# Optimization experiments

Hardware: AMD Instinct MI355X
Metric: run time of the kernel (lower is better)

Reference implementation:

```python
import jax, jax.numpy as jnp
import numpy as np

FRAME, PROJ, MID, HID, T, B = 2048, 512, 128, 1024, 48, 512


def _uniform(key, shape, stdv):
    return jax.random.uniform(key, shape, jnp.float32, -stdv, stdv)


def setup_inputs() -> dict:
    key = jax.random.key(0)
    ks = jax.random.split(key, 16)
    sp = 1.0 / np.sqrt(FRAME)   # frame_embed init
    s1 = 1.0 / np.sqrt(HID)     # LSTMCell init (1/sqrt(hidden))
    sbd = 1.0 / np.sqrt(PROJ)   # BoundaryDetector init (1/sqrt(i_features))
    return {
        "video_feats": jax.random.normal(ks[0], (B, T, FRAME), jnp.float32),
        # frame_embed: Linear(frame_size, projected_size)
        "We": _uniform(ks[1], (PROJ, FRAME), sp),
        "be": _uniform(ks[2], (PROJ,), sp),
        # lstm1: LSTMCell(projected, hidden) with bias
        "W1_ih": _uniform(ks[3], (4 * HID, PROJ), s1),
        "W1_hh": _uniform(ks[4], (4 * HID, HID), s1),
        "b1_ih": _uniform(ks[5], (4 * HID,), s1),
        "b1_hh": _uniform(ks[6], (4 * HID,), s1),
        # lstm2: LSTMCell(hidden, hidden), bias=False
        "W2_ih": _uniform(ks[7], (4 * HID, HID), s1),
        "W2_hh": _uniform(ks[8], (4 * HID, HID), s1),
        # BoundaryDetector params
        "Wsi": _uniform(ks[9], (MID, PROJ), sbd),
        "Wsh": _uniform(ks[10], (MID, HID), sbd),
        "bbd": _uniform(ks[11], (MID,), sbd),
        "vs": _uniform(ks[12], (1, MID), sbd),
    }


def _lstm_cell(x, h, c, W_ih, W_hh, b):
    gates = x @ W_ih.T + h @ W_hh.T + b  # [B, 4H]
    i, f, g, o = jnp.split(gates, 4, axis=-1)  # PyTorch gate order i,f,g,o
    i, f, o = jax.nn.sigmoid(i), jax.nn.sigmoid(f), jax.nn.sigmoid(o)
    g = jnp.tanh(g)
    c_new = f * c + i * g
    h_new = o * jnp.tanh(c_new)
    return h_new, c_new


def _binary_gate(z):
    # eval mode: threshold 0.5; straight-through identity backward
    hard = (z > 0.5).astype(z.dtype)
    return z + jax.lax.stop_gradient(hard - z)


def reference(video_feats, We, be, W1_ih, W1_hh, b1_ih, b1_hh, W2_ih, W2_hh, Wsi, Wsh, bbd, vs):
    bsz = video_feats.shape[0]
    # frame embedding (dropout is identity in eval mode)
    v = video_feats @ We.T + be  # [B, T, PROJ]
    v_t = jnp.swapaxes(v, 0, 1)  # [T, B, PROJ]
    b1 = b1_ih + b1_hh
    zeros = jnp.zeros((bsz, HID), video_feats.dtype)

    def step(carry, vt):
        h1, c1, h2, c2 = carry
        z = jax.nn.sigmoid((vt @ Wsi.T + h1 @ Wsh.T + bbd) @ vs.T)  # [B, 1]
        s = _binary_gate(z)
        h1n, c1n = _lstm_cell(vt, h1, c1, W1_ih, W1_hh, b1)
        h2n, c2n = _lstm_cell(h1n * s, h2, c2, W2_ih, W2_hh, 0.0)
        h1n = h1n * (1.0 - s)
        c1n = c1n * (1.0 - s)
        return (h1n, c1n, h2n, c2n), None

    (h1, _, _, _), _ = jax.lax.scan(step, (zeros, zeros, zeros, zeros), v_t)
    return h1
```

## Files before the change

### kernel.cpp

```cpp
#include <hip/hip_runtime.h>

#define B_     512
#define T_     48
#define FRAME_ 2048
#define PROJ_  512
#define MID_   128
#define HID_   1024
#define G4_    4096

typedef unsigned short u16;
typedef __bf16 bf16x8 __attribute__((ext_vector_type(8)));
typedef float  f32x4  __attribute__((ext_vector_type(4)));

__device__ __forceinline__ float sigmoidf_(float x) {
    return 1.0f / (1.0f + expf(-x));
}
__device__ __forceinline__ u16 f2bf_rn(float f) {
    unsigned int u = __float_as_uint(f);
    u += 0x7fffu + ((u >> 16) & 1u);
    return (u16)(u >> 16);
}
__device__ __forceinline__ float bf2f(u16 s) {
    return __uint_as_float(((unsigned int)s) << 16);
}
__device__ __forceinline__ void gld16(const void* g, void* l) {
    __builtin_amdgcn_global_load_lds((const __attribute__((address_space(1))) void*)g,
                                     (__attribute__((address_space(3))) void*)l, 16, 0, 0);
}
__device__ __forceinline__ uint4 pack8(const u16* h) {
    return make_uint4((unsigned)h[0] | ((unsigned)h[1] << 16),
                      (unsigned)h[2] | ((unsigned)h[3] << 16),
                      (unsigned)h[4] | ((unsigned)h[5] << 16),
                      (unsigned)h[6] | ((unsigned)h[7] << 16));
}

__global__ void wvec_kernel(const float* __restrict__ Wsi, const float* __restrict__ Wsh,
                            const float* __restrict__ vs,
                            double* __restrict__ wsi_vd, float* __restrict__ wsh_v)
{
    const int gid = blockIdx.x * 256 + threadIdx.x;
    if (gid < 512) {
        double s = 0.0;
        for (int mi = 0; mi < MID_; ++mi)
            s += (double)vs[mi] * (double)Wsi[(size_t)mi * PROJ_ + gid];
        wsi_vd[gid] = s;
    } else if (gid < 1536) {
        const int k = gid - 512;
        double s = 0.0;
        for (int mi = 0; mi < MID_; ++mi)
            s += (double)vs[mi] * (double)Wsh[(size_t)mi * HID_ + k];
        wsh_v[k] = (float)s;
    }
}

__global__ void cc_kernel(const float* __restrict__ be, const double* __restrict__ wsi_vd,
                          const float* __restrict__ vs, const float* __restrict__ bbd,
                          double* __restrict__ cc)
{
    __shared__ double red[256];
    const int tid = threadIdx.x;
    double s = 0.0;
    for (int p = tid; p < PROJ_; p += 256) s += (double)be[p] * wsi_vd[p];
    red[tid] = s;
    __syncthreads();
    for (int st = 128; st > 0; st >>= 1) {
        if (tid < st) red[tid] += red[tid + st];
        __syncthreads();
    }
    if (tid == 0) {
        double b = 0.0;
        for (int mi = 0; mi < MID_; ++mi) b += (double)vs[mi] * (double)bbd[mi];
        cc[0] = red[0] + b;
    }
}

__global__ void u_kernel(const float* __restrict__ We, const double* __restrict__ wsi_vd,
                         double* __restrict__ u)
{
    const int f = blockIdx.x * 256 + threadIdx.x;
    double s = 0.0;
    for (int p = 0; p < PROJ_; ++p)
        s += wsi_vd[p] * (double)We[(size_t)p * FRAME_ + f];
    u[f] = s;
}

__global__ __launch_bounds__(256)
void vidpack_kernel(const float* __restrict__ video, const double* __restrict__ u,
                    const double* __restrict__ cc,
                    u16* __restrict__ phi, u16* __restrict__ plo,
                    float* __restrict__ Lv)
{
    __shared__ double red[16][17];
    const int tid = threadIdx.x;
    const int r   = tid & 15, kq = tid >> 4;
    const int row = blockIdx.x * 16 + r;
    const float* vr = video + (size_t)row * FRAME_;
    double s = 0.0;
#pragma unroll
    for (int j = 0; j < 16; ++j) {
        const int k0 = kq * 128 + j * 8;
        const float4 a = *(const float4*)&vr[k0];
        const float4 b = *(const float4*)&vr[k0 + 4];
        const float f[8] = {a.x, a.y, a.z, a.w, b.x, b.y, b.z, b.w};
        s += (double)f[0]*u[k0+0] + (double)f[1]*u[k0+1] + (double)f[2]*u[k0+2]
           + (double)f[3]*u[k0+3] + (double)f[4]*u[k0+4] + (double)f[5]*u[k0+5]
           + (double)f[6]*u[k0+6] + (double)f[7]*u[k0+7];
        u16 h[8], l[8];
#pragma unroll
        for (int e = 0; e < 8; ++e) {
            h[e] = f2bf_rn(f[e]);
            l[e] = f2bf_rn(f[e] - bf2f(h[e]));
        }
        const int g = kq * 16 + j;
        const size_t off = ((size_t)g * 24576 + row) * 16;
        *(uint4*)((char*)phi + off) = pack8(h);
        *(uint4*)((char*)plo + off) = pack8(l);
    }
    red[r][kq] = s;
    __syncthreads();
    if (tid < 16) {
        double t = 0.0;
#pragma unroll
        for (int q = 0; q < 16; ++q) t += red[tid][q];
        const int rw = blockIdx.x * 16 + tid;
        Lv[(rw % T_) * B_ + rw / T_] = (float)(t + cc[0]);
    }
}

__global__ void wepack_kernel(const float* __restrict__ We,
                              u16* __restrict__ phi, u16* __restrict__ plo)
{
    const int kk = blockIdx.x, by = blockIdx.y, tid = threadIdx.x;
#pragma unroll
    for (int pass = 0; pass < 2; ++pass) {
        const int g = tid + pass * 256;
        const int ko = g >> 7, n = g & 127;
        const int p = by * 128 + n;
        const int k = kk * 32 + ko * 8;
        const float4 a = *(const float4*)&We[(size_t)p * FRAME_ + k];
        const float4 b = *(const float4*)&We[(size_t)p * FRAME_ + k + 4];
        const float f[8] = {a.x, a.y, a.z, a.w, b.x, b.y, b.z, b.w};
        u16 h[8], l[8];
#pragma unroll
        for (int e = 0; e < 8; ++e) {
            h[e] = f2bf_rn(f[e]);
            l[e] = f2bf_rn(f[e] - bf2f(h[e]));
        }
        const size_t off = (((size_t)by * 64 + kk) * 512 + g) * 16;
        *(uint4*)((char*)phi + off) = pack8(h);
        *(uint4*)((char*)plo + off) = pack8(l);
    }
}

__global__ void wihpack_kernel(const float* __restrict__ Wih,
                               u16* __restrict__ phi, u16* __restrict__ plo)
{
    const int kk = blockIdx.x, by = blockIdx.y, tid = threadIdx.x;
#pragma unroll
    for (int pass = 0; pass < 2; ++pass) {
        const int g = tid + pass * 256;
        const int ko = g >> 7, n = g & 127;
        const int gate = n & 3, hl = n >> 2;
        const int srow = gate * HID_ + by * 32 + hl;
        const int k = kk * 32 + ko * 8;
        const float4 a = *(const float4*)&Wih[(size_t)srow * PROJ_ + k];
        const float4 b = *(const float4*)&Wih[(size_t)srow * PROJ_ + k + 4];
        const float f[8] = {a.x, a.y, a.z, a.w, b.x, b.y, b.z, b.w};
        u16 h[8], l[8];
#pragma unroll
        for (int e = 0; e < 8; ++e) {
            h[e] = f2bf_rn(f[e]);
            l[e] = f2bf_rn(f[e] - bf2f(h[e]));
        }
        const size_t off = (((size_t)by * 16 + kk) * 512 + g) * 16;
        *(uint4*)((char*)phi + off) = pack8(h);
        *(uint4*)((char*)plo + off) = pack8(l);
    }
}

__global__ void whhpack_kernel(const float* __restrict__ Whh,
                               u16* __restrict__ phi, u16* __restrict__ plo)
{
    const int kk = blockIdx.x, by = blockIdx.y, tid = threadIdx.x;
#pragma unroll
    for (int pass = 0; pass < 2; ++pass) {
        const int g = tid + pass * 256;
        const int ko = g >> 7, n = g & 127;
        const int gate = n & 3, hl = n >> 2;
        const int srow = gate * HID_ + by * 32 + hl;
        const int k = kk * 32 + ko * 8;
        const float4 a = *(const float4*)&Whh[(size_t)srow * HID_ + k];
        const float4 b = *(const float4*)&Whh[(size_t)srow * HID_ + k + 4];
        const float f[8] = {a.x, a.y, a.z, a.w, b.x, b.y, b.z, b.w};
        u16 h[8], l[8];
#pragma unroll
        for (int e = 0; e < 8; ++e) {
            h[e] = f2bf_rn(f[e]);
            l[e] = f2bf_rn(f[e] - bf2f(h[e]));
        }
        const size_t off = (((size_t)by * 32 + kk) * 512 + g) * 16;
        *(uint4*)((char*)phi + off) = pack8(h);
        *(uint4*)((char*)plo + off) = pack8(l);
    }
}

__global__ void b1g_kernel(const float* __restrict__ bih, const float* __restrict__ bhh,
                           float* __restrict__ b1g)
{
    const int n = blockIdx.x * 256 + threadIdx.x;
    const int by = n >> 7, nl = n & 127;
    const int gate = nl & 3, hl = nl >> 2;
    const int src = gate * HID_ + by * 32 + hl;
    b1g[n] = bih[src] + bhh[src];
}


__global__ __launch_bounds__(512, 4)
void embed_mfma_kernel(const u16* __restrict__ Ahi_g, const u16* __restrict__ Alo_g,
                       const u16* __restrict__ Bhi_g, const u16* __restrict__ Blo_g,
                       const float* __restrict__ be,
                       u16* __restrict__ vphi, u16* __restrict__ vplo)
{
    __shared__ char smem[33792];
    const int tid = threadIdx.x;
    const int xcd = blockIdx.x & 7, s_ = blockIdx.x >> 3;
    const int by = s_ & 3, bx = xcd * 48 + (s_ >> 2);
    const int n0 = by * 128;
    const int w = tid >> 6, l = tid & 63, lm = l & 15, ko4 = l >> 4;
    const int wr = (w >> 2) * 32, wc = (w & 3) * 32;
    const int t8 = tid & 255;
    const int koA = t8 >> 6, am = t8 & 63;

    const char* aV = (const char*)(tid < 256 ? Ahi_g : Alo_g)
                     + (size_t)koA * 393216 + ((size_t)bx * 64 + am) * 16;
    const char* bh = (const char*)Bhi_g + (size_t)by * 524288
                     + ((size_t)(ko4 * 128 + wc + lm)) * 16;
    const char* bl = (const char*)Blo_g + (size_t)by * 524288
                     + ((size_t)(ko4 * 128 + wc + lm)) * 16;
    char* lbase = smem + (tid >> 8) * 4096 + t8 * 16;

    f32x4 acc[2][2] = {};
    bf16x8 nBh[2], nBl[2], cBh[2], cBl[2], fAh[2], fAl[2];

    gld16(aV, lbase);
    gld16(aV + 1572864, lbase + 8192);
#pragma unroll
    for (int nt = 0; nt < 2; ++nt) {
        nBh[nt] = *(const bf16x8*)(bh + nt * 256);
        nBl[nt] = *(const bf16x8*)(bl + nt * 256);
    }

#pragma unroll
    for (int kk = 0; kk < 64; ++kk) {
        if (kk == 63) asm volatile("s_waitcnt vmcnt(4)\ns_barrier" ::: "memory");
        else          asm volatile("s_waitcnt vmcnt(5)\ns_barrier" ::: "memory");
        __builtin_amdgcn_sched_barrier(0);
#pragma unroll
        for (int nt = 0; nt < 2; ++nt) { cBh[nt] = nBh[nt]; cBl[nt] = nBl[nt]; }
        const char* rb = smem + (kk & 3) * 8192;
#pragma unroll
        for (int mt = 0; mt < 2; ++mt) {
            fAh[mt] = *(const bf16x8*)(rb + (ko4 * 64 + wr + mt * 16 + lm) * 16);
            fAl[mt] = *(const bf16x8*)(rb + 4096 + (ko4 * 64 + wr + mt * 16 + lm) * 16);
        }
        if (kk + 1 < 64) {
#pragma unroll
            for (int nt = 0; nt < 2; ++nt) {
                nBh[nt] = *(const bf16x8*)(bh + (size_t)(kk + 1) * 8192 + nt * 256);
                nBl[nt] = *(const bf16x8*)(bl + (size_t)(kk + 1) * 8192 + nt * 256);
            }
        }
        if (kk + 2 < 64) gld16(aV + (size_t)(kk + 2) * 1572864, lbase + ((kk + 2) & 3) * 8192);
#pragma unroll
        for (int mt = 0; mt < 2; ++mt)
#pragma unroll
            for (int nt = 0; nt < 2; ++nt) {
                acc[mt][nt] = __builtin_amdgcn_mfma_f32_16x16x32_bf16(fAh[mt], cBh[nt], acc[mt][nt], 0, 0, 0);
                acc[mt][nt] = __builtin_amdgcn_mfma_f32_16x16x32_bf16(fAh[mt], cBl[nt], acc[mt][nt], 0, 0, 0);
                acc[mt][nt] = __builtin_amdgcn_mfma_f32_16x16x32_bf16(fAl[mt], cBh[nt], acc[mt][nt], 0, 0, 0);
            }
    }
    asm volatile("s_waitcnt lgkmcnt(0)" ::: "memory");
    __builtin_amdgcn_sched_barrier(0);

    __syncthreads();
    float* S = (float*)smem;
#pragma unroll
    for (int mt = 0; mt < 2; ++mt)
#pragma unroll
        for (int nt = 0; nt < 2; ++nt) {
            const int col = wc + nt * 16 + lm;
#pragma unroll
            for (int r = 0; r < 4; ++r) {
                const int row = wr + mt * 16 + ko4 * 4 + r;
                S[row * 132 + col] = acc[mt][nt][r];
            }
        }
    __syncthreads();

#pragma unroll
    for (int pass = 0; pass < 2; ++pass) {
        const int pidx = tid + pass * 512;
        const int m = pidx >> 4, gr = pidx & 15;
        const int p0 = n0 + gr * 8;
        const float4 s0 = *(const float4*)&S[m * 132 + gr * 8];
        const float4 s1 = *(const float4*)&S[m * 132 + gr * 8 + 4];
        const float4 e0 = *(const float4*)&be[p0];
        const float4 e1 = *(const float4*)&be[p0 + 4];
        const float o[8] = {s0.x + e0.x, s0.y + e0.y, s0.z + e0.z, s0.w + e0.w,
                            s1.x + e1.x, s1.y + e1.y, s1.z + e1.z, s1.w + e1.w};
        u16 h[8], lo[8];
#pragma unroll
        for (int e = 0; e < 8; ++e) {
            h[e] = f2bf_rn(o[e]);
            lo[e] = f2bf_rn(o[e] - bf2f(h[e]));
        }
        const int R = bx * 64 + m;
        const int t = R % T_, b = R / T_;
        const size_t off = (size_t)t * 524288 + (((size_t)(p0 >> 3)) * 512 + b) * 16;
        *(uint4*)((char*)vphi + off) = pack8(h);
        *(uint4*)((char*)vplo + off) = pack8(lo);
    }
}

__global__ __launch_bounds__(512, 4)
void gx_mfma_kernel(const u16* __restrict__ vphi, const u16* __restrict__ vplo,
                    const u16* __restrict__ Wihhi, const u16* __restrict__ Wihlo,
                    const float* __restrict__ b1g, float* __restrict__ Gx)
{
    __shared__ char smem[33792];
    const int tid = threadIdx.x;
    const int by32 = blockIdx.x & 31;
    const int tb2  = blockIdx.x >> 5;
    const int t2 = tb2 >> 3, bx2 = tb2 & 7;
    const int b02 = bx2 * 64, n02 = by32 * 128;
    const int w = tid >> 6, l = tid & 63, lm = l & 15, ko4 = l >> 4;
    const int wr = (w >> 2) * 32, wc = (w & 3) * 32;
    const int t8 = tid & 255;
    const int koA = t8 >> 6, am = t8 & 63;

    const char* aV = (const char*)(tid < 256 ? vphi : vplo)
                     + (size_t)t2 * 524288 + ((size_t)koA * 512 + b02 + am) * 16;
    const char* bh = (const char*)Wihhi + (size_t)by32 * 131072
                     + ((size_t)(ko4 * 128 + wc + lm)) * 16;
    const char* bl = (const char*)Wihlo + (size_t)by32 * 131072
                     + ((size_t)(ko4 * 128 + wc + lm)) * 16;
    char* lbase = smem + (tid >> 8) * 4096 + t8 * 16;

    f32x4 acc[2][2] = {};
    bf16x8 nBh[2], nBl[2], cBh[2], cBl[2], fAh[2], fAl[2];

    gld16(aV, lbase);
    gld16(aV + 32768, lbase + 8192);
#pragma unroll
    for (int nt = 0; nt < 2; ++nt) {
        nBh[nt] = *(const bf16x8*)(bh + nt * 256);
        nBl[nt] = *(const bf16x8*)(bl + nt * 256);
    }

#pragma unroll
    for (int kk = 0; kk < 16; ++kk) {
        if (kk == 15) asm volatile("s_waitcnt vmcnt(4)\ns_barrier" ::: "memory");
        else          asm volatile("s_waitcnt vmcnt(5)\ns_barrier" ::: "memory");
        __builtin_amdgcn_sched_barrier(0);
#pragma unroll
        for (int nt = 0; nt < 2; ++nt) { cBh[nt] = nBh[nt]; cBl[nt] = nBl[nt]; }
        const char* rb = smem + (kk & 3) * 8192;
#pragma unroll
        for (int mt = 0; mt < 2; ++mt) {
            fAh[mt] = *(const bf16x8*)(rb + (ko4 * 64 + wr + mt * 16 + lm) * 16);
            fAl[mt] = *(const bf16x8*)(rb + 4096 + (ko4 * 64 + wr + mt * 16 + lm) * 16);
        }
        if (kk + 1 < 16) {
#pragma unroll
            for (int nt = 0; nt < 2; ++nt) {
                nBh[nt] = *(const bf16x8*)(bh + (size_t)(kk + 1) * 8192 + nt * 256);
                nBl[nt] = *(const bf16x8*)(bl + (size_t)(kk + 1) * 8192 + nt * 256);
            }
        }
        if (kk + 2 < 16) gld16(aV + (size_t)(kk + 2) * 32768, lbase + ((kk + 2) & 3) * 8192);
#pragma unroll
        for (int mt = 0; mt < 2; ++mt)
#pragma unroll
            for (int nt = 0; nt < 2; ++nt) {
                acc[mt][nt] = __builtin_amdgcn_mfma_f32_16x16x32_bf16(fAh[mt], cBh[nt], acc[mt][nt], 0, 0, 0);
                acc[mt][nt] = __builtin_amdgcn_mfma_f32_16x16x32_bf16(fAh[mt], cBl[nt], acc[mt][nt], 0, 0, 0);
                acc[mt][nt] = __builtin_amdgcn_mfma_f32_16x16x32_bf16(fAl[mt], cBh[nt], acc[mt][nt], 0, 0, 0);
            }
    }
    asm volatile("s_waitcnt lgkmcnt(0)" ::: "memory");
    __builtin_amdgcn_sched_barrier(0);

    __syncthreads();
    float* S = (float*)smem;
#pragma unroll
    for (int mt = 0; mt < 2; ++mt)
#pragma unroll
        for (int nt = 0; nt < 2; ++nt) {
            const int col = wc + nt * 16 + lm;
#pragma unroll
            for (int r = 0; r < 4; ++r) {
                const int row = wr + mt * 16 + ko4 * 4 + r;
                S[row * 132 + col] = acc[mt][nt][r];
            }
        }
    __syncthreads();

#pragma unroll
    for (int pass = 0; pass < 2; ++pass) {
        const int pidx = tid + pass * 512;
        const int m = pidx >> 4, gr = pidx & 15;
        const int c0 = gr * 8;
        const float4 s0 = *(const float4*)&S[m * 132 + c0];
        const float4 s1 = *(const float4*)&S[m * 132 + c0 + 4];
        const float4 a0 = *(const float4*)&b1g[n02 + c0];
        const float4 a1 = *(const float4*)&b1g[n02 + c0 + 4];
        float* dst = Gx + ((size_t)t2 * 512 + b02 + m) * 4096 + n02 + c0;
        *(float4*)dst       = make_float4(s0.x + a0.x, s0.y + a0.y, s0.z + a0.z, s0.w + a0.w);
        *(float4*)(dst + 4) = make_float4(s1.x + a1.x, s1.y + a1.y, s1.z + a1.z, s1.w + a1.w);
    }
}

__global__ __launch_bounds__(512, 2)
void lstm_mfma_kernel(const u16* __restrict__ hhi,  const u16* __restrict__ hlo,
                      const u16* __restrict__ Whhhi, const u16* __restrict__ Whhlo,
                      const float* __restrict__ Gxt,
                      const float* __restrict__ Lv_t,
                      const float* __restrict__ Pin,
                      float* __restrict__ Pout,
                      const float* __restrict__ wsh_v,
                      float* __restrict__ c1, float* __restrict__ h1o,
                      u16* __restrict__ hhio, u16* __restrict__ hloo)
{
    __shared__ char smem[34048];
    float* keepsm = (float*)(smem + 33792);
    const int tid = threadIdx.x;
    const int bid = blockIdx.x;
    const int xcd = bid & 7, slot = bid >> 3;
    const int by  = xcd * 4 + (slot & 3);
    const int bx  = slot >> 2;
    const int b0  = bx * 64;
    const int w = tid >> 6, l = tid & 63, lm = l & 15, ko4 = l >> 4;
    const int wr = (w >> 2) * 32, wc = (w & 3) * 32;
    const int t8 = tid & 255;
    const int koA = t8 >> 6, am = t8 & 63;

    if (tid < 64) {
        double s = (double)Lv_t[b0 + tid];
#pragma unroll
        for (int j = 0; j < 32; ++j) s += (double)Pin[j * B_ + b0 + tid];
        keepsm[tid] = (s > 0.0) ? 0.0f : 1.0f;
    }

    const char* aH = (const char*)(tid < 256 ? hhi : hlo)
                     + ((size_t)koA * 512 + b0 + am) * 16;
    const char* bh = (const char*)Whhhi + (size_t)by * 262144
                     + ((size_t)(ko4 * 128 + wc + lm)) * 16;
    const char* bl = (const char*)Whhlo + (size_t)by * 262144
                     + ((size_t)(ko4 * 128 + wc + lm)) * 16;
    char* lbase = smem + (tid >> 8) * 4096 + t8 * 16;

    f32x4 acc[2][2] = {};
    bf16x8 nBh[2], nBl[2], cBh[2], cBl[2], fAh[2], fAl[2];

    gld16(aH, lbase);
    gld16(aH + 32768, lbase + 8192);
#pragma unroll
    for (int nt = 0; nt < 2; ++nt) {
        nBh[nt] = *(const bf16x8*)(bh + nt * 256);
        nBl[nt] = *(const bf16x8*)(bl + nt * 256);
    }

#pragma unroll
    for (int kk = 0; kk < 32; ++kk) {
        if (kk == 31) asm volatile("s_waitcnt vmcnt(4)\ns_barrier" ::: "memory");
        else          asm volatile("s_waitcnt vmcnt(5)\ns_barrier" ::: "memory");
        __builtin_amdgcn_sched_barrier(0);
#pragma unroll
        for (int nt = 0; nt < 2; ++nt) { cBh[nt] = nBh[nt]; cBl[nt] = nBl[nt]; }
        const char* rb = smem + (kk & 3) * 8192;
#pragma unroll
        for (int mt = 0; mt < 2; ++mt) {
            fAh[mt] = *(const bf16x8*)(rb + (ko4 * 64 + wr + mt * 16 + lm) * 16);
            fAl[mt] = *(const bf16x8*)(rb + 4096 + (ko4 * 64 + wr + mt * 16 + lm) * 16);
        }
        if (kk + 1 < 32) {
#pragma unroll
            for (int nt = 0; nt < 2; ++nt) {
                nBh[nt] = *(const bf16x8*)(bh + (size_t)(kk + 1) * 8192 + nt * 256);
                nBl[nt] = *(const bf16x8*)(bl + (size_t)(kk + 1) * 8192 + nt * 256);
            }
        }
        if (kk + 2 < 32) gld16(aH + (size_t)(kk + 2) * 32768, lbase + ((kk + 2) & 3) * 8192);
#pragma unroll
        for (int mt = 0; mt < 2; ++mt)
#pragma unroll
            for (int nt = 0; nt < 2; ++nt) {
                acc[mt][nt] = __builtin_amdgcn_mfma_f32_16x16x32_bf16(fAh[mt], cBh[nt], acc[mt][nt], 0, 0, 0);
                acc[mt][nt] = __builtin_amdgcn_mfma_f32_16x16x32_bf16(fAh[mt], cBl[nt], acc[mt][nt], 0, 0, 0);
                acc[mt][nt] = __builtin_amdgcn_mfma_f32_16x16x32_bf16(fAl[mt], cBh[nt], acc[mt][nt], 0, 0, 0);
            }
    }
    asm volatile("s_waitcnt lgkmcnt(0)" ::: "memory");
    __builtin_amdgcn_sched_barrier(0);

    const int h_l = tid & 31, rg = tid >> 5;
    const int hg  = by * 32 + h_l;
    float4 gx[4];
#pragma unroll
    for (int i = 0; i < 4; ++i)
        gx[i] = *(const float4*)&Gxt[((size_t)b0 + rg * 4 + i) * 4096 + by * 128 + h_l * 4];

    __syncthreads();
    float* S = (float*)smem;
#pragma unroll
    for (int mt = 0; mt < 2; ++mt)
#pragma unroll
        for (int nt = 0; nt < 2; ++nt) {
            const int col = wc + nt * 16 + lm;
#pragma unroll
            for (int r = 0; r < 4; ++r) {
                const int row = wr + mt * 16 + ko4 * 4 + r;
                S[row * 132 + col] = acc[mt][nt][r];
            }
        }
    __syncthreads();

    const float wv = wsh_v[hg];
    const size_t hgbase = (((size_t)by * 4 + (h_l >> 3)) * 512) * 16 + (h_l & 7) * 2;
#pragma unroll
    for (int i = 0; i < 4; ++i) {
        const int m = rg * 4 + i;
        const int b = b0 + m;
        const float4 g4 = *(const float4*)&S[m * 132 + h_l * 4];
        const float i_ = sigmoidf_(g4.x + gx[i].x);
        const float f_ = sigmoidf_(g4.y + gx[i].y);
        const float g_ = tanhf(g4.z + gx[i].z);
        const float o_ = sigmoidf_(g4.w + gx[i].w);
        const size_t off = (size_t)b * HID_ + hg;
        float cn = f_ * c1[off] + i_ * g_;
        float hn = o_ * tanhf(cn);
        const float kp = keepsm[m];
        cn *= kp; hn *= kp;
        c1[off] = cn;
        if (h1o) h1o[off] = hn;
        const u16 hb = f2bf_rn(hn);
        const size_t hoff = hgbase + (size_t)b * 16;
        *(u16*)((char*)hhio + hoff) = hb;
        *(u16*)((char*)hloo + hoff) = f2bf_rn(hn - bf2f(hb));
        float pr = hn * wv;
        pr += __shfl_xor(pr, 16);
        pr += __shfl_xor(pr, 8);
        pr += __shfl_xor(pr, 4);
        pr += __shfl_xor(pr, 2);
        pr += __shfl_xor(pr, 1);
        if (h_l == 0) Pout[by * B_ + b] = pr;
    }
}

extern "C" void kernel_launch(void* const* d_in, const int* in_sizes, int n_in,
                              void* d_out, int out_size, void* d_ws, size_t ws_size,
                              hipStream_t stream)
{
    const float* video = (const float*)d_in[0];
    const float* We    = (const float*)d_in[1];
    const float* be    = (const float*)d_in[2];
    const float* W1_ih = (const float*)d_in[3];
    const float* W1_hh = (const float*)d_in[4];
    const float* b1_ih = (const float*)d_in[5];
    const float* b1_hh = (const float*)d_in[6];
    const float* Wsi   = (const float*)d_in[9];
    const float* Wsh   = (const float*)d_in[10];
    const float* bbd   = (const float*)d_in[11];
    const float* vs    = (const float*)d_in[12];
    float* out = (float*)d_out;

    char* p = (char*)d_ws;
    auto alloc = [&](size_t bytes) { char* r = p; p += (bytes + 255) & ~(size_t)255; return r; };
    u16* vidhi = (u16*)alloc((size_t)24576 * FRAME_ * 2);
    u16* vidlo = (u16*)alloc((size_t)24576 * FRAME_ * 2);
    u16* vphi  = (u16*)alloc((size_t)T_ * B_ * PROJ_ * 2);
    u16* vplo  = (u16*)alloc((size_t)T_ * B_ * PROJ_ * 2);
    u16* Wehi  = (u16*)alloc((size_t)PROJ_ * FRAME_ * 2);
    u16* Welo  = (u16*)alloc((size_t)PROJ_ * FRAME_ * 2);
    u16* Wihhi = (u16*)alloc((size_t)G4_ * PROJ_ * 2);
    u16* Wihlo = (u16*)alloc((size_t)G4_ * PROJ_ * 2);
    u16* Whhhi = (u16*)alloc((size_t)G4_ * HID_ * 2);
    u16* Whhlo = (u16*)alloc((size_t)G4_ * HID_ * 2);
    float* Gx  = (float*)alloc((size_t)T_ * B_ * G4_ * 4);
    float* c1  = (float*)alloc((size_t)B_ * HID_ * 4);
    u16* hhiA  = (u16*)alloc((size_t)B_ * HID_ * 2);
    u16* hhiB  = (u16*)alloc((size_t)B_ * HID_ * 2);
    u16* hloA  = (u16*)alloc((size_t)B_ * HID_ * 2);
    u16* hloB  = (u16*)alloc((size_t)B_ * HID_ * 2);
    double* wsi_vd = (double*)alloc(512 * 8);
    double* ud     = (double*)alloc(2048 * 8);
    double* ccd    = (double*)alloc(256);
    float* wsh_v = (float*)alloc(1024 * 4);
    float* Lv    = (float*)alloc((size_t)T_ * B_ * 4);
    float* PA    = (float*)alloc(32 * B_ * 4);
    float* PB    = (float*)alloc(32 * B_ * 4);
    float* b1g   = (float*)alloc(G4_ * 4);

    hipMemsetAsync(c1,   0, (size_t)B_ * HID_ * 4, stream);
    hipMemsetAsync(hhiA, 0, (size_t)B_ * HID_ * 2, stream);
    hipMemsetAsync(hloA, 0, (size_t)B_ * HID_ * 2, stream);
    hipMemsetAsync(PA,   0, 32 * B_ * 4, stream);

    b1g_kernel<<<16, 256, 0, stream>>>(b1_ih, b1_hh, b1g);
    wvec_kernel<<<6, 256, 0, stream>>>(Wsi, Wsh, vs, wsi_vd, wsh_v);
    cc_kernel<<<1, 256, 0, stream>>>(be, wsi_vd, vs, bbd, ccd);
    u_kernel<<<8, 256, 0, stream>>>(We, wsi_vd, ud);
    wepack_kernel<<<dim3(64, 4), 256, 0, stream>>>(We, Wehi, Welo);
    wihpack_kernel<<<dim3(16, 32), 256, 0, stream>>>(W1_ih, Wihhi, Wihlo);
    whhpack_kernel<<<dim3(32, 32), 256, 0, stream>>>(W1_hh, Whhhi, Whhlo);
    vidpack_kernel<<<1536, 256, 0, stream>>>(video, ud, ccd, vidhi, vidlo, Lv);
    embed_mfma_kernel<<<1536, 512, 0, stream>>>(vidhi, vidlo, Wehi, Welo, be, vphi, vplo);
    gx_mfma_kernel<<<12288, 512, 0, stream>>>(vphi, vplo, Wihhi, Wihlo, b1g, Gx);

    u16* hhi_in = hhiA; u16* hhi_out = hhiB;
    u16* hlo_in = hloA; u16* hlo_out = hloB;
    float* Pin = PA; float* Pout = PB;

    for (int t = 0; t < T_; ++t) {
        float* ho = (t == T_ - 1) ? out : nullptr;
        lstm_mfma_kernel<<<256, 512, 0, stream>>>(hhi_in, hlo_in, Whhhi, Whhlo,
                                                  Gx + (size_t)t * B_ * G4_,
                                                  Lv + t * B_, Pin, Pout, wsh_v,
                                                  c1, ho, hhi_out, hlo_out);
        { u16* tmp = hhi_in; hhi_in = hhi_out; hhi_out = tmp; }
        { u16* tmp = hlo_in; hlo_in = hlo_out; hlo_out = tmp; }
        { float* tmp = Pin; Pin = Pout; Pout = tmp; }
    }
}
```

Measured before the change: 1.782 ms.

## Retile embed and Gx GEMMs to 128x128 with LDS-staged A and B

The embed and input-projection GEMMs move from 64x128 tiles on 512-thread blocks to 128x128 tiles on 256-thread blocks, each wave computing a 64x64 sub-tile. Both A and B operands are now staged through double-buffered LDS with async global loads, instead of B being read directly from global memory into registers. The Gx kernel writes results plus bias straight from registers, skipping the LDS transpose. The aim is more reuse per loaded byte and fewer redundant B fetches, at the cost of higher register and LDS use per block, which lowers occupancy.

```diff
diff --git a/kernel.cpp b/kernel.cpp
--- a/kernel.cpp
+++ b/kernel.cpp
@@ -215,210 +215,212 @@
 }
 
 
-__global__ __launch_bounds__(512, 4)
+__global__ __launch_bounds__(256, 2)
 void embed_mfma_kernel(const u16* __restrict__ Ahi_g, const u16* __restrict__ Alo_g,
                        const u16* __restrict__ Bhi_g, const u16* __restrict__ Blo_g,
                        const float* __restrict__ be,
                        u16* __restrict__ vphi, u16* __restrict__ vplo)
 {
-    __shared__ char smem[33792];
+    __shared__ char smem[65536];
     const int tid = threadIdx.x;
     const int xcd = blockIdx.x & 7, s_ = blockIdx.x >> 3;
-    const int by = s_ & 3, bx = xcd * 48 + (s_ >> 2);
-    const int n0 = by * 128;
+    const int by = s_ & 3, bx = xcd * 24 + (s_ >> 2);
+    const int n0 = by * 128, row0 = bx * 128;
     const int w = tid >> 6, l = tid & 63, lm = l & 15, ko4 = l >> 4;
-    const int wr = (w >> 2) * 32, wc = (w & 3) * 32;
-    const int t8 = tid & 255;
-    const int koA = t8 >> 6, am = t8 & 63;
-
-    const char* aV = (const char*)(tid < 256 ? Ahi_g : Alo_g)
-                     + (size_t)koA * 393216 + ((size_t)bx * 64 + am) * 16;
-    const char* bh = (const char*)Bhi_g + (size_t)by * 524288
-                     + ((size_t)(ko4 * 128 + wc + lm)) * 16;
-    const char* bl = (const char*)Blo_g + (size_t)by * 524288
-                     + ((size_t)(ko4 * 128 + wc + lm)) * 16;
-    char* lbase = smem + (tid >> 8) * 4096 + t8 * 16;
-
-    f32x4 acc[2][2] = {};
-    bf16x8 nBh[2], nBl[2], cBh[2], cBl[2], fAh[2], fAl[2];
-
-    gld16(aV, lbase);
-    gld16(aV + 1572864, lbase + 8192);
-#pragma unroll
-    for (int nt = 0; nt < 2; ++nt) {
-        nBh[nt] = *(const bf16x8*)(bh + nt * 256);
-        nBl[nt] = *(const bf16x8*)(bl + nt * 256);
-    }
-
-#pragma unroll
+    const int wr = (w >> 1) * 64, wc = (w & 1) * 64;
+
+    const char* aS[4]; const char* bS[4]; int loff[4];
+#pragma unroll
+    for (int i = 0; i < 4; ++i) {
+        const int j = w * 4 + i;
+        const int ip = (j & 7) * 64 + l;
+        const int ko = ip >> 7, rc = ip & 127;
+        const char* ab = (j >> 3) ? (const char*)Alo_g : (const char*)Ahi_g;
+        aS[i] = ab + ((size_t)ko * 24576 + row0 + rc) * 16;
+        const char* bb = (j >> 3) ? (const char*)Blo_g : (const char*)Bhi_g;
+        bS[i] = bb + (size_t)by * 524288 + (size_t)ip * 16;
+        loff[i] = j * 1024 + l * 16;
+    }
+
+    f32x4 acc[4][4] = {};
+#pragma unroll
+    for (int i = 0; i < 4; ++i) {
+        gld16(aS[i], smem + loff[i]);
+        gld16(bS[i], smem + 16384 + loff[i]);
+    }
+
+#pragma unroll 2
     for (int kk = 0; kk < 64; ++kk) {
-        if (kk == 63) asm volatile("s_waitcnt vmcnt(4)\ns_barrier" ::: "memory");
-        else          asm volatile("s_waitcnt vmcnt(5)\ns_barrier" ::: "memory");
+        if (kk + 1 < 64) {
+            const int bo = ((kk + 1) & 1) * 32768;
+#pragma unroll
+            for (int i = 0; i < 4; ++i) {
+                gld16(aS[i] + (size_t)(kk + 1) * 1572864, smem + bo + loff[i]);
+                gld16(bS[i] + (size_t)(kk + 1) * 8192,    smem + bo + 16384 + loff[i]);
+            }
+            asm volatile("s_waitcnt vmcnt(8)\ns_barrier" ::: "memory");
+        } else {
+            asm volatile("s_waitcnt vmcnt(0)\ns_barrier" ::: "memory");
+        }
         __builtin_amdgcn_sched_barrier(0);
-#pragma unroll
-        for (int nt = 0; nt < 2; ++nt) { cBh[nt] = nBh[nt]; cBl[nt] = nBl[nt]; }
-        const char* rb = smem + (kk & 3) * 8192;
-#pragma unroll
-        for (int mt = 0; mt < 2; ++mt) {
-            fAh[mt] = *(const bf16x8*)(rb + (ko4 * 64 + wr + mt * 16 + lm) * 16);
-            fAl[mt] = *(const bf16x8*)(rb + 4096 + (ko4 * 64 + wr + mt * 16 + lm) * 16);
-        }
-        if (kk + 1 < 64) {
-#pragma unroll
-            for (int nt = 0; nt < 2; ++nt) {
-                nBh[nt] = *(const bf16x8*)(bh + (size_t)(kk + 1) * 8192 + nt * 256);
-                nBl[nt] = *(const bf16x8*)(bl + (size_t)(kk + 1) * 8192 + nt * 256);
-            }
-        }
-        if (kk + 2 < 64) gld16(aV + (size_t)(kk + 2) * 1572864, lbase + ((kk + 2) & 3) * 8192);
-#pragma unroll
-        for (int mt = 0; mt < 2; ++mt)
-#pragma unroll
-            for (int nt = 0; nt < 2; ++nt) {
-                acc[mt][nt] = __builtin_amdgcn_mfma_f32_16x16x32_bf16(fAh[mt], cBh[nt], acc[mt][nt], 0, 0, 0);
-                acc[mt][nt] = __builtin_amdgcn_mfma_f32_16x16x32_bf16(fAh[mt], cBl[nt], acc[mt][nt], 0, 0, 0);
-                acc[mt][nt] = __builtin_amdgcn_mfma_f32_16x16x32_bf16(fAl[mt], cBh[nt], acc[mt][nt], 0, 0, 0);
-            }
-    }
-    asm volatile("s_waitcnt lgkmcnt(0)" ::: "memory");
-    __builtin_amdgcn_sched_barrier(0);
+
+        const char* rb = smem + (kk & 1) * 32768;
+        bf16x8 Ah[4], Al[4], Bh[4], Bl[4];
+#pragma unroll
+        for (int mt = 0; mt < 4; ++mt) {
+            const int idx = (ko4 * 128 + wr + mt * 16 + lm) * 16;
+            Ah[mt] = *(const bf16x8*)(rb + idx);
+            Al[mt] = *(const bf16x8*)(rb + 8192 + idx);
+        }
+#pragma unroll
+        for (int nt = 0; nt < 4; ++nt) {
+            const int idx = (ko4 * 128 + wc + nt * 16 + lm) * 16;
+            Bh[nt] = *(const bf16x8*)(rb + 16384 + idx);
+            Bl[nt] = *(const bf16x8*)(rb + 24576 + idx);
+        }
+        asm volatile("s_waitcnt lgkmcnt(0)\ns_barrier" ::: "memory");
+        __builtin_amdgcn_sched_barrier(0);
+#pragma unroll
+        for (int mt = 0; mt < 4; ++mt)
+#pragma unroll
+            for (int nt = 0; nt < 4; ++nt) {
+                acc[mt][nt] = __builtin_amdgcn_mfma_f32_16x16x32_bf16(Ah[mt], Bh[nt], acc[mt][nt], 0, 0, 0);
+                acc[mt][nt] = __builtin_amdgcn_mfma_f32_16x16x32_bf16(Ah[mt], Bl[nt], acc[mt][nt], 0, 0, 0);
+                acc[mt][nt] = __builtin_amdgcn_mfma_f32_16x16x32_bf16(Al[mt], Bh[nt], acc[mt][nt], 0, 0, 0);
+            }
+    }
 
     __syncthreads();
     float* S = (float*)smem;
 #pragma unroll
-    for (int mt = 0; mt < 2; ++mt)
-#pragma unroll
-        for (int nt = 0; nt < 2; ++nt) {
-            const int col = wc + nt * 16 + lm;
-#pragma unroll
-            for (int r = 0; r < 4; ++r) {
-                const int row = wr + mt * 16 + ko4 * 4 + r;
-                S[row * 132 + col] = acc[mt][nt][r];
-            }
-        }
-    __syncthreads();
-
-#pragma unroll
-    for (int pass = 0; pass < 2; ++pass) {
-        const int pidx = tid + pass * 512;
-        const int m = pidx >> 4, gr = pidx & 15;
-        const int p0 = n0 + gr * 8;
-        const float4 s0 = *(const float4*)&S[m * 132 + gr * 8];
-        const float4 s1 = *(const float4*)&S[m * 132 + gr * 8 + 4];
-        const float4 e0 = *(const float4*)&be[p0];
-        const float4 e1 = *(const float4*)&be[p0 + 4];
-        const float o[8] = {s0.x + e0.x, s0.y + e0.y, s0.z + e0.z, s0.w + e0.w,
-                            s1.x + e1.x, s1.y + e1.y, s1.z + e1.z, s1.w + e1.w};
-        u16 h[8], lo[8];
-#pragma unroll
-        for (int e = 0; e < 8; ++e) {
-            h[e] = f2bf_rn(o[e]);
-            lo[e] = f2bf_rn(o[e] - bf2f(h[e]));
-        }
-        const int R = bx * 64 + m;
-        const int t = R % T_, b = R / T_;
-        const size_t off = (size_t)t * 524288 + (((size_t)(p0 >> 3)) * 512 + b) * 16;
-        *(uint4*)((char*)vphi + off) = pack8(h);
-        *(uint4*)((char*)vplo + off) = pack8(lo);
-    }
-}
-
-__global__ __launch_bounds__(512, 4)
+    for (int h = 0; h < 2; ++h) {
+        if ((w >> 1) == h) {
+#pragma unroll
+            for (int mt = 0; mt < 4; ++mt)
+#pragma unroll
+                for (int nt = 0; nt < 4; ++nt)
+#pragma unroll
+                    for (int r = 0; r < 4; ++r)
+                        S[(mt * 16 + ko4 * 4 + r) * 132 + wc + nt * 16 + lm] = acc[mt][nt][r];
+        }
+        __syncthreads();
+#pragma unroll
+        for (int i = 0; i < 4; ++i) {
+            const int task = tid * 4 + i;
+            const int m = task >> 4, gr = task & 15;
+            const int p0 = n0 + gr * 8;
+            const float4 s0 = *(const float4*)&S[m * 132 + gr * 8];
+            const float4 s1 = *(const float4*)&S[m * 132 + gr * 8 + 4];
+            const float4 e0 = *(const float4*)&be[p0];
+            const float4 e1 = *(const float4*)&be[p0 + 4];
+            const float o[8] = {s0.x + e0.x, s0.y + e0.y, s0.z + e0.z, s0.w + e0.w,
+                                s1.x + e1.x, s1.y + e1.y, s1.z + e1.z, s1.w + e1.w};
+            u16 hb[8], lb[8];
+#pragma unroll
+            for (int e = 0; e < 8; ++e) {
+                hb[e] = f2bf_rn(o[e]);
+                lb[e] = f2bf_rn(o[e] - bf2f(hb[e]));
+            }
+            const int R = row0 + h * 64 + m;
+            const int t = R % T_, b = R / T_;
+            const size_t off = (size_t)t * 524288 + (((size_t)(p0 >> 3)) * 512 + b) * 16;
+            *(uint4*)((char*)vphi + off) = pack8(hb);
+            *(uint4*)((char*)vplo + off) = pack8(lb);
+        }
+        __syncthreads();
+    }
+}
+
+__global__ __launch_bounds__(256, 2)
 void gx_mfma_kernel(const u16* __restrict__ vphi, const u16* __restrict__ vplo,
                     const u16* __restrict__ Wihhi, const u16* __restrict__ Wihlo,
                     const float* __restrict__ b1g, float* __restrict__ Gx)
 {
-    __shared__ char smem[33792];
+    __shared__ char smem[65536];
     const int tid = threadIdx.x;
-    const int by32 = blockIdx.x & 31;
-    const int tb2  = blockIdx.x >> 5;
-    const int t2 = tb2 >> 3, bx2 = tb2 & 7;
-    const int b02 = bx2 * 64, n02 = by32 * 128;
+    const int xcd = blockIdx.x & 7, s_ = blockIdx.x >> 3;
+    const int by = s_ / 24, bx = xcd * 24 + (s_ % 24);
+    const int t2 = bx >> 2, b0 = (bx & 3) * 128;
+    const int n0 = by * 128;
     const int w = tid >> 6, l = tid & 63, lm = l & 15, ko4 = l >> 4;
-    const int wr = (w >> 2) * 32, wc = (w & 3) * 32;
-    const int t8 = tid & 255;
-    const int koA = t8 >> 6, am = t8 & 63;
-
-    const char* aV = (const char*)(tid < 256 ? vphi : vplo)
-                     + (size_t)t2 * 524288 + ((size_t)koA * 512 + b02 + am) * 16;
-    const char* bh = (const char*)Wihhi + (size_t)by32 * 131072
-                     + ((size_t)(ko4 * 128 + wc + lm)) * 16;
-    const char* bl = (const char*)Wihlo + (size_t)by32 * 131072
-                     + ((size_t)(ko4 * 128 + wc + lm)) * 16;
-    char* lbase = smem + (tid >> 8) * 4096 + t8 * 16;
-
-    f32x4 acc[2][2] = {};
-    bf16x8 nBh[2], nBl[2], cBh[2], cBl[2], fAh[2], fAl[2];
-
-    gld16(aV, lbase);
-    gld16(aV + 32768, lbase + 8192);
-#pragma unroll
-    for (int nt = 0; nt < 2; ++nt) {
-        nBh[nt] = *(const bf16x8*)(bh + nt * 256);
-        nBl[nt] = *(const bf16x8*)(bl + nt * 256);
-    }
-
-#pragma unroll
+    const int wr = (w >> 1) * 64, wc = (w & 1) * 64;
+
+    const char* aS[4]; const char* bS[4]; int loff[4];
+#pragma unroll
+    for (int i = 0; i < 4; ++i) {
+        const int j = w * 4 + i;
+        const int ip = (j & 7) * 64 + l;
+        const int ko = ip >> 7, rc = ip & 127;
+        const char* ab = ((j >> 3) ? (const char*)vplo : (const char*)vphi)
+                         + (size_t)t2 * 524288;
+        aS[i] = ab + ((size_t)ko * 512 + b0 + rc) * 16;
+        const char* bb = (j >> 3) ? (const char*)Wihlo : (const char*)Wihhi;
+        bS[i] = bb + (size_t)by * 131072 + (size_t)ip * 16;
+        loff[i] = j * 1024 + l * 16;
+    }
+
+    f32x4 acc[4][4] = {};
+#pragma unroll
+    for (int i = 0; i < 4; ++i) {
+        gld16(aS[i], smem + loff[i]);
+        gld16(bS[i], smem + 16384 + loff[i]);
+    }
+
+#pragma unroll 2
     for (int kk = 0; kk < 16; ++kk) {
-        if (kk == 15) asm volatile("s_waitcnt vmcnt(4)\ns_barrier" ::: "memory");
-        else          asm volatile("s_waitcnt vmcnt(5)\ns_barrier" ::: "memory");
+        if (kk + 1 < 16) {
+            const int bo = ((kk + 1) & 1) * 32768;
+#pragma unroll
+            for (int i = 0; i < 4; ++i) {
+                gld16(aS[i] + (size_t)(kk + 1) * 32768, smem + bo + loff[i]);
+                gld16(bS[i] + (size_t)(kk + 1) * 8192,  smem + bo + 16384 + loff[i]);
+            }
+            asm volatile("s_waitcnt vmcnt(8)\ns_barrier" ::: "memory");
+        } else {
+            asm volatile("s_waitcnt vmcnt(0)\ns_barrier" ::: "memory");
+        }
         __builtin_amdgcn_sched_barrier(0);
-#pragma unroll
-        for (int nt = 0; nt < 2; ++nt) { cBh[nt] = nBh[nt]; cBl[nt] = nBl[nt]; }
-        const char* rb = smem + (kk & 3) * 8192;
-#pragma unroll
-        for (int mt = 0; mt < 2; ++mt) {
-            fAh[mt] = *(const bf16x8*)(rb + (ko4 * 64 + wr + mt * 16 + lm) * 16);
-            fAl[mt] = *(const bf16x8*)(rb + 4096 + (ko4 * 64 + wr + mt * 16 + lm) * 16);
-        }
-        if (kk + 1 < 16) {
-#pragma unroll
-            for (int nt = 0; nt < 2; ++nt) {
-                nBh[nt] = *(const bf16x8*)(bh + (size_t)(kk + 1) * 8192 + nt * 256);
-                nBl[nt] = *(const bf16x8*)(bl + (size_t)(kk + 1) * 8192 + nt * 256);
-            }
-        }
-        if (kk + 2 < 16) gld16(aV + (size_t)(kk + 2) * 32768, lbase + ((kk + 2) & 3) * 8192);
-#pragma unroll
-        for (int mt = 0; mt < 2; ++mt)
-#pragma unroll
-            for (int nt = 0; nt < 2; ++nt) {
-                acc[mt][nt] = __builtin_amdgcn_mfma_f32_16x16x32_bf16(fAh[mt], cBh[nt], acc[mt][nt], 0, 0, 0);
-                acc[mt][nt] = __builtin_amdgcn_mfma_f32_16x16x32_bf16(fAh[mt], cBl[nt], acc[mt][nt], 0, 0, 0);
-                acc[mt][nt] = __builtin_amdgcn_mfma_f32_16x16x32_bf16(fAl[mt], cBh[nt], acc[mt][nt], 0, 0, 0);
-            }
-    }
-    asm volatile("s_waitcnt lgkmcnt(0)" ::: "memory");
-    __builtin_amdgcn_sched_barrier(0);
-
-    __syncthreads();
-    float* S = (float*)smem;
-#pragma unroll
-    for (int mt = 0; mt < 2; ++mt)
-#pragma unroll
-        for (int nt = 0; nt < 2; ++nt) {
-            const int col = wc + nt * 16 + lm;
-#pragma unroll
-            for (int r = 0; r < 4; ++r) {
-                const int row = wr + mt * 16 + ko4 * 4 + r;
-                S[row * 132 + col] = acc[mt][nt][r];
-            }
-        }
-    __syncthreads();
-
-#pragma unroll
-    for (int pass = 0; pass < 2; ++pass) {
-        const int pidx = tid + pass * 512;
-        const int m = pidx >> 4, gr = pidx & 15;
-        const int c0 = gr * 8;
-        const float4 s0 = *(const float4*)&S[m * 132 + c0];
-        const float4 s1 = *(const float4*)&S[m * 132 + c0 + 4];
-        const float4 a0 = *(const float4*)&b1g[n02 + c0];
-        const float4 a1 = *(const float4*)&b1g[n02 + c0 + 4];
-        float* dst = Gx + ((size_t)t2 * 512 + b02 + m) * 4096 + n02 + c0;
-        *(float4*)dst       = make_float4(s0.x + a0.x, s0.y + a0.y, s0.z + a0.z, s0.w + a0.w);
-        *(float4*)(dst + 4) = make_float4(s1.x + a1.x, s1.y + a1.y, s1.z + a1.z, s1.w + a1.w);
-    }
+
+        const char* rb = smem + (kk & 1) * 32768;
+        bf16x8 Ah[4], Al[4], Bh[4], Bl[4];
+#pragma unroll
+        for (int mt = 0; mt < 4; ++mt) {
+            const int idx = (ko4 * 128 + wr + mt * 16 + lm) * 16;
+            Ah[mt] = *(const bf16x8*)(rb + idx);
+            Al[mt] = *(const bf16x8*)(rb + 8192 + idx);
+        }
+#pragma unroll
+        for (int nt = 0; nt < 4; ++nt) {
+            const int idx = (ko4 * 128 + wc + nt * 16 + lm) * 16;
+            Bh[nt] = *(const bf16x8*)(rb + 16384 + idx);
+            Bl[nt] = *(const bf16x8*)(rb + 24576 + idx);
+        }
+        asm volatile("s_waitcnt lgkmcnt(0)\ns_barrier" ::: "memory");
+        __builtin_amdgcn_sched_barrier(0);
+#pragma unroll
+        for (int mt = 0; mt < 4; ++mt)
+#pragma unroll
+            for (int nt = 0; nt < 4; ++nt) {
+                acc[mt][nt] = __builtin_amdgcn_mfma_f32_16x16x32_bf16(Ah[mt], Bh[nt], acc[mt][nt], 0, 0, 0);
+                acc[mt][nt] = __builtin_amdgcn_mfma_f32_16x16x32_bf16(Ah[mt], Bl[nt], acc[mt][nt], 0, 0, 0);
+                acc[mt][nt] = __builtin_amdgcn_mfma_f32_16x16x32_bf16(Al[mt], Bh[nt], acc[mt][nt], 0, 0, 0);
+            }
+    }
+
+    float bg[4];
+#pragma unroll
+    for (int nt = 0; nt < 4; ++nt) bg[nt] = b1g[n0 + wc + nt * 16 + lm];
+    float* gbase = Gx + ((size_t)t2 * 512 + b0) * 4096 + n0;
+#pragma unroll
+    for (int mt = 0; mt < 4; ++mt)
+#pragma unroll
+        for (int r = 0; r < 4; ++r) {
+            const int row = wr + mt * 16 + ko4 * 4 + r;
+            float* rp = gbase + (size_t)row * 4096 + wc;
+#pragma unroll
+            for (int nt = 0; nt < 4; ++nt)
+                rp[nt * 16 + lm] = acc[mt][nt][r] + bg[nt];
+        }
 }
 
 __global__ __launch_bounds__(512, 2)
@@ -615,8 +617,8 @@
     wihpack_kernel<<<dim3(16, 32), 256, 0, stream>>>(W1_ih, Wihhi, Wihlo);
     whhpack_kernel<<<dim3(32, 32), 256, 0, stream>>>(W1_hh, Whhhi, Whhlo);
     vidpack_kernel<<<1536, 256, 0, stream>>>(video, ud, ccd, vidhi, vidlo, Lv);
-    embed_mfma_kernel<<<1536, 512, 0, stream>>>(vidhi, vidlo, Wehi, Welo, be, vphi, vplo);
-    gx_mfma_kernel<<<12288, 512, 0, stream>>>(vphi, vplo, Wihhi, Wihlo, b1g, Gx);
+    embed_mfma_kernel<<<768, 256, 0, stream>>>(vidhi, vidlo, Wehi, Welo, be, vphi, vplo);
+    gx_mfma_kernel<<<6144, 256, 0, stream>>>(vphi, vplo, Wihhi, Wihlo, b1g, Gx);
 
     u16* hhi_in = hhiA; u16* hhi_out = hhiB;
     u16* hlo_in = hloA; u16* hlo_out = hloB;
```

Measured after the change: 1.611 ms. 9.6% less time.
